# Kernel tuning notes

Measured on AMD Instinct MI355X. Metric: run time of the kernel, lower is better.

## Reference

```python
import jax, jax.numpy as jnp
import numpy as np

N_NODES = 100000
N_EDGES = 1600000
IN_DIM = 128
HIDDEN = 128


def setup_inputs() -> dict:
    key = jax.random.key(0)
    ks = jax.random.split(key, 8)
    x = jax.random.normal(ks[0], (N_NODES, IN_DIM), dtype=jnp.float32)
    edge_index = jax.random.randint(ks[1], (2, N_EDGES), 0, N_NODES, dtype=jnp.int32)
    # GCNConv weights (glorot-style scale) and biases
    s1 = 1.0 / np.sqrt(IN_DIM)
    s2 = 1.0 / np.sqrt(HIDDEN)
    W1 = jax.random.normal(ks[2], (IN_DIM, HIDDEN), dtype=jnp.float32) * s1
    b1 = jnp.zeros((HIDDEN,), dtype=jnp.float32)
    W2 = jax.random.normal(ks[3], (HIDDEN, HIDDEN), dtype=jnp.float32) * s2
    b2 = jnp.zeros((HIDDEN,), dtype=jnp.float32)
    Wout = jax.random.normal(ks[4], (HIDDEN, 1), dtype=jnp.float32) * s2
    bout = jnp.zeros((1,), dtype=jnp.float32)
    return {"x": x, "edge_index": edge_index, "W1": W1, "b1": b1,
            "W2": W2, "b2": b2, "Wout": Wout, "bout": bout}


def _gcn_conv(x, row, col, norm, W, b, n_nodes):
    # x' = D^-1/2 (A + I) D^-1/2 (x W) + b   (PyG GCNConv, symmetric norm)
    xw = x @ W                                   # [N, H] dense GEMM
    msg = xw[row] * norm[:, None]                # gather + scale  [E+N, H]
    out = jax.ops.segment_sum(msg, col, num_segments=n_nodes)  # scatter-add
    return out + b


def reference(x, edge_index, W1, b1, W2, b2, Wout, bout):
    n = x.shape[0]
    self_idx = jnp.arange(n, dtype=edge_index.dtype)
    row = jnp.concatenate([edge_index[0], self_idx])   # sources (+ self loops)
    col = jnp.concatenate([edge_index[1], self_idx])   # targets (+ self loops)
    deg = jax.ops.segment_sum(jnp.ones_like(col, x.dtype), col, num_segments=n)
    dis = jax.lax.rsqrt(deg)                            # deg >= 1 (self loops)
    norm = dis[row] * dis[col]                          # [E+N]
    h = jax.nn.relu(_gcn_conv(x, row, col, norm, W1, b1, n))
    h = jax.nn.relu(_gcn_conv(h, row, col, norm, W2, b2, n))
    # mlp_layers=1 -> empty Sequential; dropout identity at inference
    return (h @ Wout + bout).squeeze(-1)                # [N]
```

## Files before the change

kernel.cpp:

```cpp
#include <hip/hip_runtime.h>


typedef __attribute__((ext_vector_type(8))) short bf16x8;
typedef __attribute__((ext_vector_type(4))) float f32x4;
typedef _Float16 half4 __attribute__((ext_vector_type(4)));

__device__ __forceinline__ unsigned short bf16_rn(float f) {
  unsigned u = __builtin_bit_cast(unsigned, f);
  u += 0x7FFFu + ((u >> 16) & 1u);
  return (unsigned short)(u >> 16);
}

__global__ __launch_bounds__(256) void fill_k(const int* __restrict__ row,
                                              const int* __restrict__ col,
                                              int* __restrict__ cnt,
                                              int* __restrict__ bkt,
                                              int E, int N) {
  int g = blockIdx.x & 7;
  int bg = blockIdx.x >> 3;
  int bpg = gridDim.x >> 3;
  int nd8 = N >> 3;
  int lo = g * nd8, hi = lo + nd8;
  int chunk = (E + bpg - 1) / bpg;
  int e0 = bg * chunk;
  int e1 = e0 + chunk; if (e1 > E) e1 = E;
  for (int e = e0 + threadIdx.x; e < e1; e += 256) {
    int c = col[e];
    if (c >= lo && c < hi) {
      int r = row[e];
      int pos = atomicAdd(&cnt[c], 1);
      if (pos < 64) bkt[(size_t)c * 64 + pos] = r;
    }
  }
}

__global__ void dis_k(const int* __restrict__ cnt, float* __restrict__ dis, int n) {
  int i = blockIdx.x * blockDim.x + threadIdx.x;
  if (i < n) dis[i] = rsqrtf((float)(cnt[i] + 1));
}

__global__ void wprep_k(const float* __restrict__ W, short* __restrict__ wh,
                        short* __restrict__ wl) {
  int t = blockIdx.x * 256 + threadIdx.x;
  int j = t & 7, l = (t >> 3) & 63, ct = (t >> 9) & 7, ks = t >> 12;
  int k = ks * 32 + ((l >> 4) * 8) + j;
  int c = ct * 16 + (l & 15);
  float w = W[k * 128 + c];
  unsigned short h = bf16_rn(w);
  float hf = __builtin_bit_cast(float, (unsigned)h << 16);
  wh[t] = (short)h;
  wl[t] = (short)bf16_rn(w - hf);
}

__global__ __launch_bounds__(256) void gemm_mfma_k(const float* __restrict__ A,
                                                   const short* __restrict__ whp,
                                                   const short* __restrict__ wlp,
                                                   const float* __restrict__ dis,
                                                   _Float16* __restrict__ Y, int n) {
  int lane = threadIdx.x & 63;
  int wave = threadIdx.x >> 6;
  long row0 = ((long)blockIdx.x * 4 + wave) * 16;
  if (row0 >= n) return;
  int mr = lane & 15, kg = lane >> 4;
  const float* arow = A + (row0 + mr) * 128 + kg * 8;
  const bf16x8* WH = (const bf16x8*)whp;
  const bf16x8* WL = (const bf16x8*)wlp;
  f32x4 acc[8];
#pragma unroll
  for (int ct = 0; ct < 8; ++ct) acc[ct] = (f32x4){0.f, 0.f, 0.f, 0.f};
#pragma unroll
  for (int ks = 0; ks < 4; ++ks) {
    float4 a0 = *(const float4*)(arow + ks * 32);
    float4 a1 = *(const float4*)(arow + ks * 32 + 4);
    float av[8] = {a0.x, a0.y, a0.z, a0.w, a1.x, a1.y, a1.z, a1.w};
    bf16x8 ah, al;
#pragma unroll
    for (int j = 0; j < 8; ++j) {
      unsigned short h = bf16_rn(av[j]);
      float hf = __builtin_bit_cast(float, (unsigned)h << 16);
      ah[j] = (short)h;
      al[j] = (short)bf16_rn(av[j] - hf);
    }
#pragma unroll
    for (int ct = 0; ct < 8; ++ct) {
      bf16x8 bh = WH[(ks * 8 + ct) * 64 + lane];
      bf16x8 bl = WL[(ks * 8 + ct) * 64 + lane];
      acc[ct] = __builtin_amdgcn_mfma_f32_16x16x32_bf16(ah, bh, acc[ct], 0, 0, 0);
      acc[ct] = __builtin_amdgcn_mfma_f32_16x16x32_bf16(al, bh, acc[ct], 0, 0, 0);
      acc[ct] = __builtin_amdgcn_mfma_f32_16x16x32_bf16(ah, bl, acc[ct], 0, 0, 0);
    }
  }
  float sc[4];
#pragma unroll
  for (int j = 0; j < 4; ++j) sc[j] = dis[row0 + kg * 4 + j];
  _Float16* crow = Y + (row0 + kg * 4) * 128 + mr;
#pragma unroll
  for (int ct = 0; ct < 8; ++ct)
#pragma unroll
    for (int j = 0; j < 4; ++j)
      crow[(size_t)j * 128 + ct * 16] = (_Float16)(acc[ct][j] * sc[j]);
}

__device__ __forceinline__ float4 agg_core(const half4* __restrict__ Y,
                                           const int* __restrict__ cnt,
                                           const int* __restrict__ bkt,
                                           int c, int r) {
  int m = cnt[c]; if (m > 64) m = 64;
  int idxA = (r < m) ? bkt[(size_t)c * 64 + r] : 0;
  half4 sv = Y[(size_t)c * 32 + r];
  float4 acc = make_float4((float)sv[0], (float)sv[1], (float)sv[2], (float)sv[3]);
  int mA = m < 32 ? m : 32;
  int j = 0;
  for (; j + 8 <= mA; j += 8) {
    half4 v[8];
#pragma unroll
    for (int q = 0; q < 8; ++q) {
      int s = __shfl(idxA, j + q, 32);
      v[q] = Y[(size_t)s * 32 + r];
    }
#pragma unroll
    for (int q = 0; q < 8; ++q) {
      acc.x += (float)v[q][0]; acc.y += (float)v[q][1];
      acc.z += (float)v[q][2]; acc.w += (float)v[q][3];
    }
  }
  for (; j < mA; ++j) {
    int s = __shfl(idxA, j, 32);
    half4 v = Y[(size_t)s * 32 + r];
    acc.x += (float)v[0]; acc.y += (float)v[1];
    acc.z += (float)v[2]; acc.w += (float)v[3];
  }
  if (m > 32) {
    int idxB = (32 + r < m) ? bkt[(size_t)c * 64 + 32 + r] : 0;
    for (j = 32; j < m; ++j) {
      int s = __shfl(idxB, j - 32, 32);
      half4 v = Y[(size_t)s * 32 + r];
      acc.x += (float)v[0]; acc.y += (float)v[1];
      acc.z += (float)v[2]; acc.w += (float)v[3];
    }
  }
  return acc;
}

__global__ __launch_bounds__(256) void agg_mid_k(const _Float16* __restrict__ y,
                                                 const float* __restrict__ dis,
                                                 const int* __restrict__ cnt,
                                                 const int* __restrict__ bkt,
                                                 const float* __restrict__ bias,
                                                 float* __restrict__ h, int n) {
  int c = (blockIdx.x * 256 + threadIdx.x) >> 5;
  if (c >= n) return;
  int r = threadIdx.x & 31;
  float4 acc = agg_core((const half4*)y, cnt, bkt, c, r);
  float d = dis[c];
  float4 b = *(const float4*)&bias[r * 4];
  float4 o;
  o.x = fmaxf(fmaf(acc.x, d, b.x), 0.f);
  o.y = fmaxf(fmaf(acc.y, d, b.y), 0.f);
  o.z = fmaxf(fmaf(acc.z, d, b.z), 0.f);
  o.w = fmaxf(fmaf(acc.w, d, b.w), 0.f);
  *(float4*)&h[(size_t)c * 128 + r * 4] = o;
}

__global__ __launch_bounds__(256) void agg_final_k(const _Float16* __restrict__ y,
                                                   const float* __restrict__ dis,
                                                   const int* __restrict__ cnt,
                                                   const int* __restrict__ bkt,
                                                   const float* __restrict__ bias,
                                                   const float* __restrict__ Wout,
                                                   const float* __restrict__ bout,
                                                   float* __restrict__ out, int n) {
  int c = (blockIdx.x * 256 + threadIdx.x) >> 5;
  if (c >= n) return;
  int r = threadIdx.x & 31;
  float4 acc = agg_core((const half4*)y, cnt, bkt, c, r);
  float d = dis[c];
  float4 b = *(const float4*)&bias[r * 4];
  float4 w4 = *(const float4*)&Wout[r * 4];
  float hx = fmaxf(fmaf(acc.x, d, b.x), 0.f);
  float hy = fmaxf(fmaf(acc.y, d, b.y), 0.f);
  float hz = fmaxf(fmaf(acc.z, d, b.z), 0.f);
  float hw = fmaxf(fmaf(acc.w, d, b.w), 0.f);
  float partial = hx * w4.x + hy * w4.y + hz * w4.z + hw * w4.w;
#pragma unroll
  for (int off = 16; off > 0; off >>= 1) partial += __shfl_down(partial, off, 32);
  if (r == 0) out[c] = partial + bout[0];
}

extern "C" void kernel_launch(void* const* d_in, const int* in_sizes, int n_in,
                              void* d_out, int out_size, void* d_ws, size_t ws_size,
                              hipStream_t stream) {
  const float* x    = (const float*)d_in[0];
  const int*   ei   = (const int*)d_in[1];
  const float* W1   = (const float*)d_in[2];
  const float* b1   = (const float*)d_in[3];
  const float* W2   = (const float*)d_in[4];
  const float* b2   = (const float*)d_in[5];
  const float* Wout = (const float*)d_in[6];
  const float* bout = (const float*)d_in[7];
  float* out = (float*)d_out;

  const int N = in_sizes[0] / 128;
  const int E = in_sizes[1] / 2;
  const int* row = ei;
  const int* col = ei + E;

  char* ws = (char*)d_ws;
  size_t cur = 0;
  auto alloc = [&](size_t bytes) -> void* {
    cur = (cur + 255) & ~(size_t)255;
    void* p = ws + cur;
    cur += bytes;
    return p;
  };
  _Float16* y   = (_Float16*)alloc((size_t)N * 128 * 2);
  float*    h   = (float*)alloc((size_t)N * 128 * 4);
  int*      bkt = (int*)alloc((size_t)N * 64 * 4);
  int*      cnt = (int*)alloc((size_t)N * 4);
  float*    dis = (float*)alloc((size_t)N * 4);
  short*    wh1 = (short*)alloc(16384 * 2);
  short*    wl1 = (short*)alloc(16384 * 2);
  short*    wh2 = (short*)alloc(16384 * 2);
  short*    wl2 = (short*)alloc(16384 * 2);
  (void)ws_size; (void)n_in; (void)out_size;

  const int gN = (N + 255) / 256;
  const int gGemm = (N + 63) / 64;
  const int gAgg = (N + 7) / 8;

  wprep_k<<<64, 256, 0, stream>>>(W1, wh1, wl1);
  wprep_k<<<64, 256, 0, stream>>>(W2, wh2, wl2);

  hipMemsetAsync(cnt, 0, (size_t)N * 4, stream);
  fill_k<<<2048, 256, 0, stream>>>(row, col, cnt, bkt, E, N);
  dis_k<<<gN, 256, 0, stream>>>(cnt, dis, N);

  gemm_mfma_k<<<gGemm, 256, 0, stream>>>(x, wh1, wl1, dis, y, N);
  agg_mid_k<<<gAgg, 256, 0, stream>>>(y, dis, cnt, bkt, b1, h, N);

  gemm_mfma_k<<<gGemm, 256, 0, stream>>>(h, wh2, wl2, dis, y, N);
  agg_final_k<<<gAgg, 256, 0, stream>>>(y, dis, cnt, bkt, b2, Wout, bout, out, N);
}
```

Before: 344.7 us.

## Store GEMM output in column-blocked layout and aggregate per feature block

The GEMM now writes Y as 8 column blocks of 16 features each ([8][N][16] fp16). The aggregation kernels assign each block group to one feature slice, so the gathered working set per slice (N*32 bytes) is more likely to stay cache-resident. Each wave processes one node, with 8 lanes per edge and 8 edges in flight, and reduces across lanes with xor shuffles. The final layer writes per-block partial dot products and adds a small reduce kernel, and nontemporal loads/stores are added on streaming data. In exchange, the bucket index list is re-read once per feature block, the gathers become narrower 4-byte loads, and one extra launch is added.

```diff
diff --git a/kernel.cpp b/kernel.cpp
--- a/kernel.cpp
+++ b/kernel.cpp
@@ -3,7 +3,8 @@
 
 typedef __attribute__((ext_vector_type(8))) short bf16x8;
 typedef __attribute__((ext_vector_type(4))) float f32x4;
-typedef _Float16 half4 __attribute__((ext_vector_type(4)));
+typedef __attribute__((ext_vector_type(2))) float f32x2;
+typedef _Float16 f16x2 __attribute__((ext_vector_type(2)));
 
 __device__ __forceinline__ unsigned short bf16_rn(float f) {
   unsigned u = __builtin_bit_cast(unsigned, f);
@@ -25,9 +26,9 @@
   int e0 = bg * chunk;
   int e1 = e0 + chunk; if (e1 > E) e1 = E;
   for (int e = e0 + threadIdx.x; e < e1; e += 256) {
-    int c = col[e];
+    int c = __builtin_nontemporal_load(col + e);
     if (c >= lo && c < hi) {
-      int r = row[e];
+      int r = __builtin_nontemporal_load(row + e);
       int pos = atomicAdd(&cnt[c], 1);
       if (pos < 64) bkt[(size_t)c * 64 + pos] = r;
     }
@@ -70,9 +71,9 @@
   for (int ct = 0; ct < 8; ++ct) acc[ct] = (f32x4){0.f, 0.f, 0.f, 0.f};
 #pragma unroll
   for (int ks = 0; ks < 4; ++ks) {
-    float4 a0 = *(const float4*)(arow + ks * 32);
-    float4 a1 = *(const float4*)(arow + ks * 32 + 4);
-    float av[8] = {a0.x, a0.y, a0.z, a0.w, a1.x, a1.y, a1.z, a1.w};
+    f32x4 a0 = __builtin_nontemporal_load((const f32x4*)(arow + ks * 32));
+    f32x4 a1 = __builtin_nontemporal_load((const f32x4*)(arow + ks * 32 + 4));
+    float av[8] = {a0[0], a0[1], a0[2], a0[3], a1[0], a1[1], a1[2], a1[3]};
     bf16x8 ah, al;
 #pragma unroll
     for (int j = 0; j < 8; ++j) {
@@ -93,98 +94,108 @@
   float sc[4];
 #pragma unroll
   for (int j = 0; j < 4; ++j) sc[j] = dis[row0 + kg * 4 + j];
-  _Float16* crow = Y + (row0 + kg * 4) * 128 + mr;
-#pragma unroll
-  for (int ct = 0; ct < 8; ++ct)
+#pragma unroll
+  for (int ct = 0; ct < 8; ++ct) {
+    _Float16* yb = Y + ((size_t)ct * n + row0 + kg * 4) * 16 + mr;
 #pragma unroll
     for (int j = 0; j < 4; ++j)
-      crow[(size_t)j * 128 + ct * 16] = (_Float16)(acc[ct][j] * sc[j]);
-}
-
-__device__ __forceinline__ float4 agg_core(const half4* __restrict__ Y,
+      yb[(size_t)j * 16] = (_Float16)(acc[ct][j] * sc[j]);
+  }
+}
+
+__device__ __forceinline__ f32x2 agg_edges(const _Float16* __restrict__ ys,
                                            const int* __restrict__ cnt,
                                            const int* __restrict__ bkt,
-                                           int c, int r) {
+                                           int c, int lane, int q, int fp) {
   int m = cnt[c]; if (m > 64) m = 64;
-  int idxA = (r < m) ? bkt[(size_t)c * 64 + r] : 0;
-  half4 sv = Y[(size_t)c * 32 + r];
-  float4 acc = make_float4((float)sv[0], (float)sv[1], (float)sv[2], (float)sv[3]);
-  int mA = m < 32 ? m : 32;
-  int j = 0;
-  for (; j + 8 <= mA; j += 8) {
-    half4 v[8];
-#pragma unroll
-    for (int q = 0; q < 8; ++q) {
-      int s = __shfl(idxA, j + q, 32);
-      v[q] = Y[(size_t)s * 32 + r];
-    }
-#pragma unroll
-    for (int q = 0; q < 8; ++q) {
-      acc.x += (float)v[q][0]; acc.y += (float)v[q][1];
-      acc.z += (float)v[q][2]; acc.w += (float)v[q][3];
-    }
-  }
-  for (; j < mA; ++j) {
-    int s = __shfl(idxA, j, 32);
-    half4 v = Y[(size_t)s * 32 + r];
-    acc.x += (float)v[0]; acc.y += (float)v[1];
-    acc.z += (float)v[2]; acc.w += (float)v[3];
-  }
-  if (m > 32) {
-    int idxB = (32 + r < m) ? bkt[(size_t)c * 64 + 32 + r] : 0;
-    for (j = 32; j < m; ++j) {
-      int s = __shfl(idxB, j - 32, 32);
-      half4 v = Y[(size_t)s * 32 + r];
-      acc.x += (float)v[0]; acc.y += (float)v[1];
-      acc.z += (float)v[2]; acc.w += (float)v[3];
-    }
-  }
-  return acc;
-}
-
-__global__ __launch_bounds__(256) void agg_mid_k(const _Float16* __restrict__ y,
+  int idxA = 0;
+  if (lane < m) idxA = __builtin_nontemporal_load(&bkt[(size_t)c * 64 + lane]);
+  float ax = 0.f, ay = 0.f;
+  for (int j = 0; j < m; j += 8) {
+    int jj = j + q;
+    int s = __shfl(idxA, jj);
+    if (jj < m) {
+      f16x2 v = *(const f16x2*)&ys[(size_t)s * 16 + fp * 2];
+      ax += (float)v[0]; ay += (float)v[1];
+    }
+  }
+  ax += __shfl_xor(ax, 8);  ay += __shfl_xor(ay, 8);
+  ax += __shfl_xor(ax, 16); ay += __shfl_xor(ay, 16);
+  ax += __shfl_xor(ax, 32); ay += __shfl_xor(ay, 32);
+  f16x2 sv = *(const f16x2*)&ys[(size_t)c * 16 + fp * 2];
+  f32x2 r;
+  r[0] = ax + (float)sv[0];
+  r[1] = ay + (float)sv[1];
+  return r;
+}
+
+__global__ __launch_bounds__(256) void agg_mid_k(const _Float16* __restrict__ yblk,
                                                  const float* __restrict__ dis,
                                                  const int* __restrict__ cnt,
                                                  const int* __restrict__ bkt,
                                                  const float* __restrict__ bias,
                                                  float* __restrict__ h, int n) {
-  int c = (blockIdx.x * 256 + threadIdx.x) >> 5;
-  if (c >= n) return;
-  int r = threadIdx.x & 31;
-  float4 acc = agg_core((const half4*)y, cnt, bkt, c, r);
-  float d = dis[c];
-  float4 b = *(const float4*)&bias[r * 4];
-  float4 o;
-  o.x = fmaxf(fmaf(acc.x, d, b.x), 0.f);
-  o.y = fmaxf(fmaf(acc.y, d, b.y), 0.f);
-  o.z = fmaxf(fmaf(acc.z, d, b.z), 0.f);
-  o.w = fmaxf(fmaf(acc.w, d, b.w), 0.f);
-  *(float4*)&h[(size_t)c * 128 + r * 4] = o;
-}
-
-__global__ __launch_bounds__(256) void agg_final_k(const _Float16* __restrict__ y,
+  int g = blockIdx.x & 7;
+  int bg = blockIdx.x >> 3;
+  int w = threadIdx.x >> 6, lane = threadIdx.x & 63;
+  int q = lane >> 3, fp = lane & 7;
+  const _Float16* ys = yblk + (size_t)g * n * 16;
+  f32x2 b2 = *(const f32x2*)&bias[g * 16 + fp * 2];
+#pragma unroll
+  for (int t = 0; t < 4; ++t) {
+    int c = bg * 16 + w * 4 + t;
+    if (c >= n) break;
+    f32x2 acc = agg_edges(ys, cnt, bkt, c, lane, q, fp);
+    if (q == 0) {
+      float d = dis[c];
+      f32x2 o;
+      o[0] = fmaxf(fmaf(acc[0], d, b2[0]), 0.f);
+      o[1] = fmaxf(fmaf(acc[1], d, b2[1]), 0.f);
+      __builtin_nontemporal_store(o, (f32x2*)&h[(size_t)c * 128 + g * 16 + fp * 2]);
+    }
+  }
+}
+
+__global__ __launch_bounds__(256) void agg_final_k(const _Float16* __restrict__ yblk,
                                                    const float* __restrict__ dis,
                                                    const int* __restrict__ cnt,
                                                    const int* __restrict__ bkt,
                                                    const float* __restrict__ bias,
                                                    const float* __restrict__ Wout,
-                                                   const float* __restrict__ bout,
-                                                   float* __restrict__ out, int n) {
-  int c = (blockIdx.x * 256 + threadIdx.x) >> 5;
-  if (c >= n) return;
-  int r = threadIdx.x & 31;
-  float4 acc = agg_core((const half4*)y, cnt, bkt, c, r);
-  float d = dis[c];
-  float4 b = *(const float4*)&bias[r * 4];
-  float4 w4 = *(const float4*)&Wout[r * 4];
-  float hx = fmaxf(fmaf(acc.x, d, b.x), 0.f);
-  float hy = fmaxf(fmaf(acc.y, d, b.y), 0.f);
-  float hz = fmaxf(fmaf(acc.z, d, b.z), 0.f);
-  float hw = fmaxf(fmaf(acc.w, d, b.w), 0.f);
-  float partial = hx * w4.x + hy * w4.y + hz * w4.z + hw * w4.w;
-#pragma unroll
-  for (int off = 16; off > 0; off >>= 1) partial += __shfl_down(partial, off, 32);
-  if (r == 0) out[c] = partial + bout[0];
+                                                   float* __restrict__ partial, int n) {
+  int g = blockIdx.x & 7;
+  int bg = blockIdx.x >> 3;
+  int w = threadIdx.x >> 6, lane = threadIdx.x & 63;
+  int q = lane >> 3, fp = lane & 7;
+  const _Float16* ys = yblk + (size_t)g * n * 16;
+  f32x2 b2 = *(const f32x2*)&bias[g * 16 + fp * 2];
+  f32x2 w2 = *(const f32x2*)&Wout[g * 16 + fp * 2];
+#pragma unroll
+  for (int t = 0; t < 4; ++t) {
+    int c = bg * 16 + w * 4 + t;
+    if (c >= n) break;
+    f32x2 acc = agg_edges(ys, cnt, bkt, c, lane, q, fp);
+    float d = dis[c];
+    float hx = fmaxf(fmaf(acc[0], d, b2[0]), 0.f);
+    float hy = fmaxf(fmaf(acc[1], d, b2[1]), 0.f);
+    float p = hx * w2[0] + hy * w2[1];
+    p += __shfl_xor(p, 1);
+    p += __shfl_xor(p, 2);
+    p += __shfl_xor(p, 4);
+    if (lane == 0) partial[(size_t)g * n + c] = p;
+  }
+}
+
+__global__ void reduce_k(const float* __restrict__ partial,
+                         const float* __restrict__ bout,
+                         float* __restrict__ out, int n) {
+  int c = blockIdx.x * 256 + threadIdx.x;
+  if (c < n) {
+    float s = bout[0];
+#pragma unroll
+    for (int g = 0; g < 8; ++g) s += partial[(size_t)g * n + c];
+    out[c] = s;
+  }
 }
 
 extern "C" void kernel_launch(void* const* d_in, const int* in_sizes, int n_in,
@@ -213,31 +224,33 @@
     cur += bytes;
     return p;
   };
-  _Float16* y   = (_Float16*)alloc((size_t)N * 128 * 2);
-  float*    h   = (float*)alloc((size_t)N * 128 * 4);
-  int*      bkt = (int*)alloc((size_t)N * 64 * 4);
-  int*      cnt = (int*)alloc((size_t)N * 4);
-  float*    dis = (float*)alloc((size_t)N * 4);
-  short*    wh1 = (short*)alloc(16384 * 2);
-  short*    wl1 = (short*)alloc(16384 * 2);
-  short*    wh2 = (short*)alloc(16384 * 2);
-  short*    wl2 = (short*)alloc(16384 * 2);
+  _Float16* yblk = (_Float16*)alloc((size_t)N * 128 * 2);
+  float*    h    = (float*)alloc((size_t)N * 128 * 4);
+  int*      bkt  = (int*)alloc((size_t)N * 64 * 4);
+  int*      cnt  = (int*)alloc((size_t)N * 4);
+  float*    dis  = (float*)alloc((size_t)N * 4);
+  float*    part = (float*)alloc((size_t)N * 8 * 4);
+  short*    wh1  = (short*)alloc(16384 * 2);
+  short*    wl1  = (short*)alloc(16384 * 2);
+  short*    wh2  = (short*)alloc(16384 * 2);
+  short*    wl2  = (short*)alloc(16384 * 2);
   (void)ws_size; (void)n_in; (void)out_size;
 
   const int gN = (N + 255) / 256;
   const int gGemm = (N + 63) / 64;
-  const int gAgg = (N + 7) / 8;
+  const int gAgg = ((N + 15) / 16) * 8;
 
   wprep_k<<<64, 256, 0, stream>>>(W1, wh1, wl1);
   wprep_k<<<64, 256, 0, stream>>>(W2, wh2, wl2);
 
-  hipMemsetAsync(cnt, 0, (size_t)N * 4, stream);
+  (void)hipMemsetAsync(cnt, 0, (size_t)N * 4, stream);
   fill_k<<<2048, 256, 0, stream>>>(row, col, cnt, bkt, E, N);
   dis_k<<<gN, 256, 0, stream>>>(cnt, dis, N);
 
-  gemm_mfma_k<<<gGemm, 256, 0, stream>>>(x, wh1, wl1, dis, y, N);
-  agg_mid_k<<<gAgg, 256, 0, stream>>>(y, dis, cnt, bkt, b1, h, N);
-
-  gemm_mfma_k<<<gGemm, 256, 0, stream>>>(h, wh2, wl2, dis, y, N);
-  agg_final_k<<<gAgg, 256, 0, stream>>>(y, dis, cnt, bkt, b2, Wout, bout, out, N);
-}
+  gemm_mfma_k<<<gGemm, 256, 0, stream>>>(x, wh1, wl1, dis, yblk, N);
+  agg_mid_k<<<gAgg, 256, 0, stream>>>(yblk, dis, cnt, bkt, b1, h, N);
+
+  gemm_mfma_k<<<gGemm, 256, 0, stream>>>(h, wh2, wl2, dis, yblk, N);
+  agg_final_k<<<gAgg, 256, 0, stream>>>(yblk, dis, cnt, bkt, b2, Wout, part, N);
+  reduce_k<<<gN, 256, 0, stream>>>(part, bout, out, N);
+}
```

New measurement: 808.7 us. 135% more time.

## Stage GEMM output through LDS for coalesced stores, add nontemporal loads

Applied to the files above, without the earlier changes.

The GEMM epilogue now writes each wave's 16x128 fp16 tile into shared memory, then stores it back to global memory as contiguous 16-byte vectors instead of scattered 2-byte stores. Streaming reads of the edge lists, the GEMM A rows and the bucket indices become nontemporal loads, to cut cache pollution and leave more cache for the gathered Y rows. The LDS round trip is synchronised only with s_waitcnt and no barrier. That holds within one wave, but it depends on the compiler not reordering the accesses.

```diff
diff --git a/kernel.cpp b/kernel.cpp
--- a/kernel.cpp
+++ b/kernel.cpp
@@ -3,7 +3,9 @@
 
 typedef __attribute__((ext_vector_type(8))) short bf16x8;
 typedef __attribute__((ext_vector_type(4))) float f32x4;
-typedef _Float16 half4 __attribute__((ext_vector_type(4)));
+typedef _Float16 f16x2 __attribute__((ext_vector_type(2)));
+typedef _Float16 f16x4 __attribute__((ext_vector_type(4)));
+typedef _Float16 f16x8 __attribute__((ext_vector_type(8)));
 
 __device__ __forceinline__ unsigned short bf16_rn(float f) {
   unsigned u = __builtin_bit_cast(unsigned, f);
@@ -25,9 +27,9 @@
   int e0 = bg * chunk;
   int e1 = e0 + chunk; if (e1 > E) e1 = E;
   for (int e = e0 + threadIdx.x; e < e1; e += 256) {
-    int c = col[e];
+    int c = __builtin_nontemporal_load(col + e);
     if (c >= lo && c < hi) {
-      int r = row[e];
+      int r = __builtin_nontemporal_load(row + e);
       int pos = atomicAdd(&cnt[c], 1);
       if (pos < 64) bkt[(size_t)c * 64 + pos] = r;
     }
@@ -57,6 +59,7 @@
                                                    const short* __restrict__ wlp,
                                                    const float* __restrict__ dis,
                                                    _Float16* __restrict__ Y, int n) {
+  __shared__ _Float16 lds[4][16][136];
   int lane = threadIdx.x & 63;
   int wave = threadIdx.x >> 6;
   long row0 = ((long)blockIdx.x * 4 + wave) * 16;
@@ -70,9 +73,9 @@
   for (int ct = 0; ct < 8; ++ct) acc[ct] = (f32x4){0.f, 0.f, 0.f, 0.f};
 #pragma unroll
   for (int ks = 0; ks < 4; ++ks) {
-    float4 a0 = *(const float4*)(arow + ks * 32);
-    float4 a1 = *(const float4*)(arow + ks * 32 + 4);
-    float av[8] = {a0.x, a0.y, a0.z, a0.w, a1.x, a1.y, a1.z, a1.w};
+    f32x4 a0 = __builtin_nontemporal_load((const f32x4*)(arow + ks * 32));
+    f32x4 a1 = __builtin_nontemporal_load((const f32x4*)(arow + ks * 32 + 4));
+    float av[8] = {a0[0], a0[1], a0[2], a0[3], a1[0], a1[1], a1[2], a1[3]};
     bf16x8 ah, al;
 #pragma unroll
     for (int j = 0; j < 8; ++j) {
@@ -93,26 +96,34 @@
   float sc[4];
 #pragma unroll
   for (int j = 0; j < 4; ++j) sc[j] = dis[row0 + kg * 4 + j];
-  _Float16* crow = Y + (row0 + kg * 4) * 128 + mr;
+  _Float16* tile = &lds[wave][0][0];
 #pragma unroll
   for (int ct = 0; ct < 8; ++ct)
 #pragma unroll
     for (int j = 0; j < 4; ++j)
-      crow[(size_t)j * 128 + ct * 16] = (_Float16)(acc[ct][j] * sc[j]);
-}
-
-__device__ __forceinline__ float4 agg_core(const half4* __restrict__ Y,
+      tile[(kg * 4 + j) * 136 + ct * 16 + mr] = (_Float16)(acc[ct][j] * sc[j]);
+  __builtin_amdgcn_s_waitcnt(0);
+  int r = lane >> 2, cq = lane & 3;
+  const _Float16* src = &tile[r * 136 + cq * 32];
+  _Float16* dst = Y + (row0 + r) * 128 + cq * 32;
+#pragma unroll
+  for (int i = 0; i < 4; ++i)
+    *(f16x8*)(dst + i * 8) = *(const f16x8*)(src + i * 8);
+}
+
+__device__ __forceinline__ float4 agg_core(const f16x4* __restrict__ Y,
                                            const int* __restrict__ cnt,
                                            const int* __restrict__ bkt,
                                            int c, int r) {
   int m = cnt[c]; if (m > 64) m = 64;
-  int idxA = (r < m) ? bkt[(size_t)c * 64 + r] : 0;
-  half4 sv = Y[(size_t)c * 32 + r];
+  int idxA = 0;
+  if (r < m) idxA = __builtin_nontemporal_load(&bkt[(size_t)c * 64 + r]);
+  f16x4 sv = Y[(size_t)c * 32 + r];
   float4 acc = make_float4((float)sv[0], (float)sv[1], (float)sv[2], (float)sv[3]);
   int mA = m < 32 ? m : 32;
   int j = 0;
   for (; j + 8 <= mA; j += 8) {
-    half4 v[8];
+    f16x4 v[8];
 #pragma unroll
     for (int q = 0; q < 8; ++q) {
       int s = __shfl(idxA, j + q, 32);
@@ -126,15 +137,16 @@
   }
   for (; j < mA; ++j) {
     int s = __shfl(idxA, j, 32);
-    half4 v = Y[(size_t)s * 32 + r];
+    f16x4 v = Y[(size_t)s * 32 + r];
     acc.x += (float)v[0]; acc.y += (float)v[1];
     acc.z += (float)v[2]; acc.w += (float)v[3];
   }
   if (m > 32) {
-    int idxB = (32 + r < m) ? bkt[(size_t)c * 64 + 32 + r] : 0;
+    int idxB = 0;
+    if (32 + r < m) idxB = __builtin_nontemporal_load(&bkt[(size_t)c * 64 + 32 + r]);
     for (j = 32; j < m; ++j) {
       int s = __shfl(idxB, j - 32, 32);
-      half4 v = Y[(size_t)s * 32 + r];
+      f16x4 v = Y[(size_t)s * 32 + r];
       acc.x += (float)v[0]; acc.y += (float)v[1];
       acc.z += (float)v[2]; acc.w += (float)v[3];
     }
@@ -151,7 +163,7 @@
   int c = (blockIdx.x * 256 + threadIdx.x) >> 5;
   if (c >= n) return;
   int r = threadIdx.x & 31;
-  float4 acc = agg_core((const half4*)y, cnt, bkt, c, r);
+  float4 acc = agg_core((const f16x4*)y, cnt, bkt, c, r);
   float d = dis[c];
   float4 b = *(const float4*)&bias[r * 4];
   float4 o;
@@ -173,7 +185,7 @@
   int c = (blockIdx.x * 256 + threadIdx.x) >> 5;
   if (c >= n) return;
   int r = threadIdx.x & 31;
-  float4 acc = agg_core((const half4*)y, cnt, bkt, c, r);
+  float4 acc = agg_core((const f16x4*)y, cnt, bkt, c, r);
   float d = dis[c];
   float4 b = *(const float4*)&bias[r * 4];
   float4 w4 = *(const float4*)&Wout[r * 4];
@@ -231,7 +243,7 @@
   wprep_k<<<64, 256, 0, stream>>>(W1, wh1, wl1);
   wprep_k<<<64, 256, 0, stream>>>(W2, wh2, wl2);
 
-  hipMemsetAsync(cnt, 0, (size_t)N * 4, stream);
+  (void)hipMemsetAsync(cnt, 0, (size_t)N * 4, stream);
   fill_k<<<2048, 256, 0, stream>>>(row, col, cnt, bkt, E, N);
   dis_k<<<gN, 256, 0, stream>>>(cnt, dis, N);
 
```

Measured after the change: 364.6 us. 1.06x slower.
